# Kernel optimization log

Measured on AMD Instinct MI355X. Metric: run time of the kernel, lower is better.

Reference implementation:

```python
import jax, jax.numpy as jnp
import numpy as np

B, N, DIM, H, GH, DH, M, L, VOCAB = 2048, 15, 512, 8, 4, 64, 256, 12, 1024
FF_IN, FF_HID = 4096, 2048  # GLU: w1 512->4096 (chunk 2), w2 2048->512


def fixed_pos_emb(n, d):
    # performer_pytorch FixedPositionalEmbedding: cat(sin, cos) along feature dim
    inv_freq = 1.0 / (10000.0 ** (jnp.arange(0, d, 2, dtype=jnp.float32) / d))
    sinu = jnp.arange(n, dtype=jnp.float32)[:, None] * inv_freq[None, :]
    return jnp.concatenate([jnp.sin(sinu), jnp.cos(sinu)], axis=-1)  # [n, d]


def layernorm(x, g, b, eps=1e-5):
    mu = x.mean(-1, keepdims=True)
    var = x.var(-1, keepdims=True)
    return (x - mu) / jnp.sqrt(var + eps) * g + b


def pre_shift(x):
    # PreShiftTokens with shifts (-1, 0, 1); feats_per_shift = 512 // 3 = 170, remainder 2 dims untouched
    fps = x.shape[-1] // 3
    s0, s1, s2, rest = x[..., :fps], x[..., fps:2 * fps], x[..., 2 * fps:3 * fps], x[..., 3 * fps:]
    pad = jnp.zeros_like(s0[:, :1])
    left = jnp.concatenate([s0[:, 1:], pad], axis=1)    # shift -1 (toward past)
    right = jnp.concatenate([pad, s2[:, :-1]], axis=1)  # shift +1
    return jnp.concatenate([left, s1, right, rest], axis=-1)


def rotate_every_two(x):
    x1, x2 = x[..., ::2], x[..., 1::2]
    return jnp.stack([-x2, x1], axis=-1).reshape(x.shape)


def apply_rotary_global(q, k, sinu):
    # performer_pytorch apply_rotary_pos_emb: sinu = cat(sin, cos); interleaved repeat
    dh = sinu.shape[-1]
    sin = jnp.repeat(sinu[:, :dh // 2], 2, axis=-1)
    cos = jnp.repeat(sinu[:, dh // 2:], 2, axis=-1)
    rot = lambda t: t * cos + rotate_every_two(t) * sin
    return rot(q), rot(k)


def softmax_kernel(x, proj, is_query, eps=1e-4):
    # FAVOR+ positive random features for softmax kernel
    d = x.shape[-1]
    dn = d ** -0.25
    ratio = proj.shape[0] ** -0.5
    dash = jnp.einsum('bhnd,md->bhnm', x * dn, proj)
    diag = 0.5 * (dn ** 2) * jnp.sum(x * x, axis=-1, keepdims=True)
    if is_query:
        mx = jnp.max(dash, axis=-1, keepdims=True)
    else:
        mx = jnp.max(dash, axis=(-1, -2), keepdims=True)
    return ratio * (jnp.exp(dash - diag - mx) + eps)


def linear_attention(q, k, v):
    # non-causal O(n) attention: q,k are [b,h,n,m] features, v [b,h,n,e]
    k_sum = k.sum(axis=-2)
    d_inv = 1.0 / jnp.einsum('bhnm,bhm->bhn', q, k_sum)
    ctx = jnp.einsum('bhnm,bhne->bhme', k, v)
    return jnp.einsum('bhme,bhnm,bhn->bhne', ctx, q, d_inv)


def local_rotary(q, k):
    # local-attention lib SinusoidalEmbeddings + rotate_half convention
    d, n = q.shape[-1], q.shape[-2]
    inv_freq = 1.0 / (10000.0 ** (jnp.arange(0, d, 2, dtype=jnp.float32) / d))
    freqs = jnp.arange(n, dtype=jnp.float32)[:, None] * inv_freq[None, :]
    freqs = jnp.concatenate([freqs, freqs], axis=-1)  # [n, d]
    cos, sin = jnp.cos(freqs), jnp.sin(freqs)
    def rot_half(x):
        x1, x2 = x[..., :d // 2], x[..., d // 2:]
        return jnp.concatenate([-x2, x1], axis=-1)
    rot = lambda t: t * cos + rot_half(t) * sin
    return rot(q), rot(k)


def self_attention(x, wq, wk, wv, wo, bo, proj, sinu):
    b, n, _ = x.shape
    to_heads = lambda W: jnp.einsum('bnd,de->bne', x, W).reshape(b, n, H, DH).transpose(0, 2, 1, 3)
    q, k, v = to_heads(wq), to_heads(wk), to_heads(wv)
    # global (FAVOR+) heads first, then local heads
    qg, kg, vg = q[:, :GH], k[:, :GH], v[:, :GH]
    ql, kl, vl = q[:, GH:], k[:, GH:], v[:, GH:]
    qg, kg = apply_rotary_global(qg, kg, sinu)
    qp = softmax_kernel(qg, proj, True)
    kp = softmax_kernel(kg, proj, False)
    out_g = linear_attention(qp, kp, vg)
    # local attention: window 256 >= n=15 and bidirectional => exact softmax over real tokens
    ql, kl = local_rotary(ql, kl)
    sim = jnp.einsum('bhid,bhjd->bhij', ql, kl) * (DH ** -0.5)
    out_l = jnp.einsum('bhij,bhjd->bhid', jax.nn.softmax(sim, axis=-1), vl)
    out = jnp.concatenate([out_g, out_l], axis=1).transpose(0, 2, 1, 3).reshape(b, n, H * DH)
    return jnp.einsum('bnd,de->bne', out, wo) + bo


def glu_ff(x, w1, b1, w2, b2):
    h = jnp.einsum('bnd,df->bnf', x, w1) + b1
    a, g = jnp.split(h, 2, axis=-1)
    return jnp.einsum('bnf,fd->bnd', jax.nn.gelu(a, approximate=False) * g, w2) + b2


def _forward(x_mcc, token_emb, ln1_g, ln1_b, Wq, Wk, Wv, Wo, bo, proj,
             ln2_g, ln2_b, W1, b1, W2, b2, lnf_g, lnf_b, Wout, bout,
             Wl1, bl1, Wl2, bl2):
    b, n = x_mcc.shape
    x = token_emb[x_mcc] + fixed_pos_emb(n, DIM)[None]  # token + absolute sinusoidal emb
    sinu = fixed_pos_emb(n, DH)                          # per-layer rotary table

    def step(carry, p):
        x1, x2 = carry
        g1, be1, wq, wk, wv, wo, bo_, pr, g2, be2, w1, bf1, w2, bf2 = p
        # reversible block: y1 = x1 + f(x2); y2 = x2 + g(y1); f/g = LN -> token-shift -> fn
        y1 = x1 + self_attention(pre_shift(layernorm(x2, g1, be1)), wq, wk, wv, wo, bo_, pr, sinu)
        y2 = x2 + glu_ff(pre_shift(layernorm(y1, g2, be2)), w1, bf1, w2, bf2)
        return (y1, y2), None

    (x1, x2), _ = jax.lax.scan(
        step, (x, x),
        (ln1_g, ln1_b, Wq, Wk, Wv, Wo, bo, proj, ln2_g, ln2_b, W1, b1, W2, b2))
    x = x1 + x2  # ReversibleSequence: sum of the two streams
    x = layernorm(x, lnf_g, lnf_b)
    logits = jnp.einsum('bnd,dv->bnv', x, Wout) + bout  # [B, N, VOCAB]
    xa = logits.mean(axis=1)
    h = jax.nn.relu(xa @ Wl1 + bl1)
    return h @ Wl2 + bl2  # [B, 2]


def _gaussian_orth(m, d, rng):
    # gaussian_orthogonal_random_matrix with scaling=0
    blocks = []
    for _ in range(m // d + 1):
        qm, _ = np.linalg.qr(rng.standard_normal((d, d)))
        blocks.append(qm.T)
    mat = np.concatenate(blocks, axis=0)[:m]
    mult = np.linalg.norm(rng.standard_normal((m, d)), axis=1)
    return (mult[:, None] * mat).astype(np.float32)


def setup_inputs():
    key = jax.random.key(0)
    ks = jax.random.split(key, 16)
    s = 0.02
    rng = np.random.default_rng(0)
    proj = jnp.asarray(np.stack([_gaussian_orth(M, DH, rng) for _ in range(L)]))
    inp = {
        'x_mcc': jax.random.randint(ks[0], (B, N), 0, VOCAB, dtype=jnp.int32).astype(jnp.int64) if False else jax.random.randint(ks[0], (B, N), 0, VOCAB),
        'token_emb': jax.random.normal(ks[1], (VOCAB, DIM), jnp.float32) * s,
        'ln1_g': jnp.ones((L, DIM), jnp.float32),
        'ln1_b': jnp.zeros((L, DIM), jnp.float32),
        'Wq': jax.random.normal(ks[2], (L, DIM, H * DH), jnp.float32) * s,
        'Wk': jax.random.normal(ks[3], (L, DIM, H * DH), jnp.float32) * s,
        'Wv': jax.random.normal(ks[4], (L, DIM, H * DH), jnp.float32) * s,
        'Wo': jax.random.normal(ks[5], (L, H * DH, DIM), jnp.float32) * s,
        'bo': jnp.zeros((L, DIM), jnp.float32),
        'proj': proj,
        'ln2_g': jnp.ones((L, DIM), jnp.float32),
        'ln2_b': jnp.zeros((L, DIM), jnp.float32),
        'W1': jax.random.normal(ks[6], (L, DIM, FF_IN), jnp.float32) * s,
        'b1': jnp.zeros((L, FF_IN), jnp.float32),
        'W2': jax.random.normal(ks[7], (L, FF_HID, DIM), jnp.float32) * s,
        'b2': jnp.zeros((L, DIM), jnp.float32),
        'lnf_g': jnp.ones((DIM,), jnp.float32),
        'lnf_b': jnp.zeros((DIM,), jnp.float32),
        'Wout': jax.random.normal(ks[8], (DIM, VOCAB), jnp.float32) * s,
        'bout': jnp.zeros((VOCAB,), jnp.float32),
        'Wl1': jax.random.normal(ks[9], (VOCAB, 64), jnp.float32) * s,
        'bl1': jnp.zeros((64,), jnp.float32),
        'Wl2': jax.random.normal(ks[10], (64, 2), jnp.float32) * s,
        'bl2': jnp.zeros((2,), jnp.float32),
    }
    return inp


def reference(x_mcc, token_emb, ln1_g, ln1_b, Wq, Wk, Wv, Wo, bo, proj,
              ln2_g, ln2_b, W1, b1, W2, b2, lnf_g, lnf_b, Wout, bout,
              Wl1, bl1, Wl2, bl2):
    return _forward(x_mcc, token_emb, ln1_g, ln1_b, Wq, Wk, Wv, Wo, bo, proj,
                    ln2_g, ln2_b, W1, b1, W2, b2, lnf_g, lnf_b, Wout, bout,
                    Wl1, bl1, Wl2, bl2)
```

## Files before the change

kernel.cpp:

```cpp
#include <hip/hip_runtime.h>
#include <math.h>

#define BB 2048
#define NN 15
#define DIMM 512
#define NH 8
#define GHH 4
#define DHH 64
#define MF 256
#define NLAYERS 12
#define NVOCAB 1024
#define ROWS (BB*NN)
#define RT (ROWS/128)

typedef __attribute__((ext_vector_type(8))) short s8b;
typedef __attribute__((ext_vector_type(4))) short s4b;
typedef __attribute__((ext_vector_type(4))) float f4;
typedef unsigned short ushort;
typedef unsigned int uint;

__device__ __forceinline__ ushort f2b(float f) {
    uint u = __builtin_bit_cast(uint, f);
    u = u + 0x7FFF + ((u >> 16) & 1);
    return (ushort)(u >> 16);
}
__device__ __forceinline__ float b2f(ushort b) {
    return __builtin_bit_cast(float, (uint)b << 16);
}
__device__ __forceinline__ void gll16(const ushort* g, ushort* l) {
    __builtin_amdgcn_global_load_lds(
        (const __attribute__((address_space(1))) uint*)g,
        (__attribute__((address_space(3))) uint*)l, 16, 0, 0);
}

__global__ __launch_bounds__(256) void k_embed(const int* __restrict__ xm,
                                               const float* __restrict__ emb,
                                               float* __restrict__ x1,
                                               float* __restrict__ x2) {
    int idx = blockIdx.x * 256 + threadIdx.x;
    int row = idx >> 9;
    int d   = idx & 511;
    int n   = row % NN;
    int tok = xm[row];
    int j   = d & 255;
    float invf = expf(-(float)j * (9.2103403720f / 256.f));
    float arg  = (float)n * invf;
    float pe   = (d < 256) ? sinf(arg) : cosf(arg);
    float val  = emb[tok * DIMM + d] + pe;
    x1[idx] = val;
    x2[idx] = val;
}

template<int SHIFT, int ADD>
__global__ __launch_bounds__(256) void k_ln(const float* __restrict__ src,
                                            const float* __restrict__ src2,
                                            const float* __restrict__ gg,
                                            const float* __restrict__ bb,
                                            ushort* __restrict__ dst) {
    __shared__ float buf[NN][DIMM];
    int b    = blockIdx.x;
    int tid  = threadIdx.x;
    int wid  = tid >> 6;
    int lane = tid & 63;

    for (int n = wid; n < NN; n += 4) {
        size_t base = ((size_t)(b * NN + n)) * DIMM;
        float4 v0 = *(const float4*)(src + base + lane * 8);
        float4 v1 = *(const float4*)(src + base + lane * 8 + 4);
        if (ADD) {
            float4 w0 = *(const float4*)(src2 + base + lane * 8);
            float4 w1 = *(const float4*)(src2 + base + lane * 8 + 4);
            v0.x += w0.x; v0.y += w0.y; v0.z += w0.z; v0.w += w0.w;
            v1.x += w1.x; v1.y += w1.y; v1.z += w1.z; v1.w += w1.w;
        }
        float s = v0.x + v0.y + v0.z + v0.w + v1.x + v1.y + v1.z + v1.w;
        #pragma unroll
        for (int m = 1; m < 64; m <<= 1) s += __shfl_xor(s, m);
        float mu = s * (1.f / DIMM);
        float a0 = v0.x - mu, a1 = v0.y - mu, a2 = v0.z - mu, a3 = v0.w - mu;
        float a4 = v1.x - mu, a5 = v1.y - mu, a6 = v1.z - mu, a7 = v1.w - mu;
        float s2 = a0*a0 + a1*a1 + a2*a2 + a3*a3 + a4*a4 + a5*a5 + a6*a6 + a7*a7;
        #pragma unroll
        for (int m = 1; m < 64; m <<= 1) s2 += __shfl_xor(s2, m);
        float rstd = 1.f / sqrtf(s2 * (1.f / DIMM) + 1e-5f);
        float o[8] = {a0, a1, a2, a3, a4, a5, a6, a7};
        int d0 = lane * 8;
        #pragma unroll
        for (int i = 0; i < 8; ++i) {
            float val = o[i] * rstd * gg[d0 + i] + bb[d0 + i];
            if (SHIFT) buf[n][d0 + i] = val;
            else       dst[base + d0 + i] = f2b(val);
        }
    }
    if (SHIFT) {
        __syncthreads();
        for (int idx = tid; idx < NN * DIMM; idx += 256) {
            int n = idx >> 9, d = idx & 511;
            float val;
            if (d < 170)      val = (n < NN - 1) ? buf[n + 1][d] : 0.f;
            else if (d < 340) val = buf[n][d];
            else if (d < 510) val = (n > 0) ? buf[n - 1][d] : 0.f;
            else              val = buf[n][d];
            dst[((size_t)(b * NN + n)) * DIMM + d] = f2b(val);
        }
    }
}

__global__ __launch_bounds__(256) void k_wt(const float* __restrict__ src,
                                            ushort* __restrict__ dst, int K, int N) {
    __shared__ float t[32][33];
    int n0 = blockIdx.x * 32, k0 = blockIdx.y * 32;
    int tx = threadIdx.x & 31, ty = threadIdx.x >> 5;
    #pragma unroll
    for (int i = 0; i < 32; i += 8)
        t[ty + i][tx] = src[(size_t)(k0 + ty + i) * N + n0 + tx];
    __syncthreads();
    #pragma unroll
    for (int i = 0; i < 32; i += 8)
        dst[(size_t)(n0 + ty + i) * K + k0 + tx] = f2b(t[tx][ty + i]);
}

__global__ __launch_bounds__(256) void k_projcvt(const float* __restrict__ src,
                                                 ushort* __restrict__ dst, int n) {
    int i = blockIdx.x * 256 + threadIdx.x;
    if (i < n) dst[i] = f2b(src[i]);
}

template<int OUTB, int BIAS, int RES>
__global__ __launch_bounds__(256) void k_mm(const ushort* __restrict__ A,
                                            const ushort* __restrict__ Bt,
                                            const float* __restrict__ bias,
                                            const float* __restrict__ res,
                                            void* __restrict__ outv,
                                            int lda, int ldb, int K, int ldo) {
    __shared__ ushort smA[128 * 32];
    __shared__ ushort smB[128 * 32];
    int tid = threadIdx.x, wid = tid >> 6, lane = tid & 63;
    int row0 = blockIdx.x * 128, col0 = blockIdx.y * 128;
    int trow = tid >> 2, tkk = (tid & 3) * 8;
    f4 acc[4][4] = {};
    int rw = (wid >> 1) * 64, cw = (wid & 1) * 64;

    for (int k0 = 0; k0 < K; k0 += 32) {
        #pragma unroll
        for (int r = 0; r < 2; ++r) {
            gll16(A  + (size_t)(row0 + r * 64 + trow) * lda + k0 + tkk, smA + (r * 256 + wid * 64) * 8);
            gll16(Bt + (size_t)(col0 + r * 64 + trow) * ldb + k0 + tkk, smB + (r * 256 + wid * 64) * 8);
        }
        __syncthreads();
        s8b af[4], bf[4];
        #pragma unroll
        for (int m = 0; m < 4; ++m)
            af[m] = *(const s8b*)(smA + (rw + m * 16 + (lane & 15)) * 32 + (lane >> 4) * 8);
        #pragma unroll
        for (int n = 0; n < 4; ++n)
            bf[n] = *(const s8b*)(smB + (cw + n * 16 + (lane & 15)) * 32 + (lane >> 4) * 8);
        #pragma unroll
        for (int m = 0; m < 4; ++m)
            #pragma unroll
            for (int n = 0; n < 4; ++n)
                acc[m][n] = __builtin_amdgcn_mfma_f32_16x16x32_bf16(af[m], bf[n], acc[m][n], 0, 0, 0);
        __syncthreads();
    }
    #pragma unroll
    for (int m = 0; m < 4; ++m) {
        #pragma unroll
        for (int n = 0; n < 4; ++n) {
            int c = col0 + cw + n * 16 + (lane & 15);
            #pragma unroll
            for (int j = 0; j < 4; ++j) {
                int r = row0 + rw + m * 16 + (lane >> 4) * 4 + j;
                float v = acc[m][n][j];
                if (BIAS) v += bias[c];
                if (RES)  v += res[(size_t)r * ldo + c];
                if (OUTB) ((ushort*)outv)[(size_t)r * ldo + c] = f2b(v);
                else      ((float*)outv)[(size_t)r * ldo + c] = v;
            }
        }
    }
}

__global__ __launch_bounds__(256) void k_glu(const ushort* __restrict__ A,
                                             const ushort* __restrict__ Ba,
                                             const ushort* __restrict__ Bg,
                                             const float* __restrict__ ba,
                                             const float* __restrict__ bg,
                                             ushort* __restrict__ outp) {
    __shared__ ushort smA[128 * 32];
    __shared__ ushort smBa[128 * 32];
    __shared__ ushort smBg[128 * 32];
    int tid = threadIdx.x, wid = tid >> 6, lane = tid & 63;
    int row0 = blockIdx.x * 128, col0 = blockIdx.y * 128;
    int trow = tid >> 2, tkk = (tid & 3) * 8;
    f4 acca[4][4] = {}, accg[4][4] = {};
    int rw = (wid >> 1) * 64, cw = (wid & 1) * 64;

    for (int k0 = 0; k0 < 512; k0 += 32) {
        #pragma unroll
        for (int r = 0; r < 2; ++r) {
            gll16(A  + (size_t)(row0 + r * 64 + trow) * 512 + k0 + tkk, smA  + (r * 256 + wid * 64) * 8);
            gll16(Ba + (size_t)(col0 + r * 64 + trow) * 512 + k0 + tkk, smBa + (r * 256 + wid * 64) * 8);
            gll16(Bg + (size_t)(col0 + r * 64 + trow) * 512 + k0 + tkk, smBg + (r * 256 + wid * 64) * 8);
        }
        __syncthreads();
        s8b af[4], bfa[4], bfg[4];
        #pragma unroll
        for (int m = 0; m < 4; ++m)
            af[m] = *(const s8b*)(smA + (rw + m * 16 + (lane & 15)) * 32 + (lane >> 4) * 8);
        #pragma unroll
        for (int n = 0; n < 4; ++n) {
            bfa[n] = *(const s8b*)(smBa + (cw + n * 16 + (lane & 15)) * 32 + (lane >> 4) * 8);
            bfg[n] = *(const s8b*)(smBg + (cw + n * 16 + (lane & 15)) * 32 + (lane >> 4) * 8);
        }
        #pragma unroll
        for (int m = 0; m < 4; ++m)
            #pragma unroll
            for (int n = 0; n < 4; ++n) {
                acca[m][n] = __builtin_amdgcn_mfma_f32_16x16x32_bf16(af[m], bfa[n], acca[m][n], 0, 0, 0);
                accg[m][n] = __builtin_amdgcn_mfma_f32_16x16x32_bf16(af[m], bfg[n], accg[m][n], 0, 0, 0);
            }
        __syncthreads();
    }
    #pragma unroll
    for (int m = 0; m < 4; ++m) {
        #pragma unroll
        for (int n = 0; n < 4; ++n) {
            int c = col0 + cw + n * 16 + (lane & 15);
            float biasa = ba[c], biasg = bg[c];
            #pragma unroll
            for (int j = 0; j < 4; ++j) {
                int r = row0 + rw + m * 16 + (lane >> 4) * 4 + j;
                float a = acca[m][n][j] + biasa;
                float g = accg[m][n][j] + biasg;
                float ge = 0.5f * a * (1.f + erff(a * 0.70710678118f));
                outp[(size_t)r * 1024 + c] = f2b(ge * g);
            }
        }
    }
}

__global__ __launch_bounds__(256) void k_attng(const ushort* __restrict__ qkv,
                                               const ushort* __restrict__ projb,
                                               ushort* __restrict__ outp) {
    __shared__ ushort sxq[16][72];
    __shared__ ushort sxk[16][72];
    __shared__ ushort sVT[64][40];
    __shared__ ushort sqp[16][264];
    __shared__ ushort skp[16][264];
    __shared__ ushort sA[16][40];
    __shared__ float sdq[16], sdk[16], sdinv[16];
    __shared__ float sPq[4][16];
    __shared__ float sPk[4];
    int b = blockIdx.x, h = blockIdx.y;
    int tid = threadIdx.x, w = tid >> 6, l = tid & 63;
    int i16 = l & 15, g = l >> 4;
    const ushort* basep = qkv + (size_t)b * NN * 1536 + h * 64;

    {
        uint* z1 = (uint*)&sVT[0][0];
        for (int i = tid; i < 1280; i += 256) z1[i] = 0;
        uint* z2 = (uint*)&sA[0][0];
        for (int i = tid; i < 320; i += 256) z2[i] = 0;
        if (tid < 64) { sxq[15][tid] = 0; sxk[15][tid] = 0; }
    }
    __syncthreads();
    for (int idx = tid; idx < NN * 32; idx += 256) {
        int n = idx >> 5, i = idx & 31;
        float invf = expf(-(float)i * (9.2103403720f / 32.f));
        float cc = cosf((float)n * invf), ss = sinf((float)n * invf);
        float q0 = b2f(basep[n * 1536 + 2 * i]), q1 = b2f(basep[n * 1536 + 2 * i + 1]);
        sxq[n][2 * i]     = f2b(q0 * cc - q1 * ss);
        sxq[n][2 * i + 1] = f2b(q1 * cc + q0 * ss);
        float k0 = b2f(basep[n * 1536 + 512 + 2 * i]), k1 = b2f(basep[n * 1536 + 512 + 2 * i + 1]);
        sxk[n][2 * i]     = f2b(k0 * cc - k1 * ss);
        sxk[n][2 * i + 1] = f2b(k1 * cc + k0 * ss);
    }
    for (int idx = tid; idx < NN * 64; idx += 256) {
        int n = idx >> 6, e = idx & 63;
        sVT[e][n] = basep[n * 1536 + 1024 + e];
    }
    __syncthreads();
    if (w == 0) {
        int n = l >> 2, c = l & 3;
        float sa = 0.f, sb = 0.f;
        #pragma unroll
        for (int s = 0; s < 2; ++s) {
            s8b vq = *(const s8b*)&sxq[n][c * 16 + s * 8];
            s8b vk = *(const s8b*)&sxk[n][c * 16 + s * 8];
            #pragma unroll
            for (int j = 0; j < 8; ++j) {
                float x = b2f((ushort)vq[j]); sa += x * x;
                float y = b2f((ushort)vk[j]); sb += y * y;
            }
        }
        sa += __shfl_xor(sa, 1); sa += __shfl_xor(sa, 2);
        sb += __shfl_xor(sb, 1); sb += __shfl_xor(sb, 2);
        if (c == 0) { sdq[n] = 0.0625f * sa; sdk[n] = 0.0625f * sb; }
    }
    s8b bq[2], bk[2];
    bq[0] = *(const s8b*)&sxq[i16][g * 8];
    bq[1] = *(const s8b*)&sxq[i16][32 + g * 8];
    bk[0] = *(const s8b*)&sxk[i16][g * 8];
    bk[1] = *(const s8b*)&sxk[i16][32 + g * 8];
    f4 accq[4] = {}, acck[4] = {};
    const ushort* pb = projb + (size_t)(w * 64 + i16) * 64 + g * 8;
    #pragma unroll
    for (int mi = 0; mi < 4; ++mi) {
        #pragma unroll
        for (int ks = 0; ks < 2; ++ks) {
            s8b a = *(const s8b*)(pb + mi * 16 * 64 + ks * 32);
            accq[mi] = __builtin_amdgcn_mfma_f32_16x16x32_bf16(a, bq[ks], accq[mi], 0, 0, 0);
            acck[mi] = __builtin_amdgcn_mfma_f32_16x16x32_bf16(a, bk[ks], acck[mi], 0, 0, 0);
        }
    }
    float mq = -1e30f, mkv = -1e30f;
    #pragma unroll
    for (int mi = 0; mi < 4; ++mi)
        #pragma unroll
        for (int j = 0; j < 4; ++j) {
            mq  = fmaxf(mq, accq[mi][j]);
            mkv = fmaxf(mkv, acck[mi][j]);
        }
    if (i16 == 15) mkv = -1e30f;
    mq = fmaxf(mq, __shfl_xor(mq, 16));
    mq = fmaxf(mq, __shfl_xor(mq, 32));
    #pragma unroll
    for (int m = 1; m < 64; m <<= 1) mkv = fmaxf(mkv, __shfl_xor(mkv, m));
    if (l < 16) sPq[w][l] = mq;
    if (l == 0) sPk[w] = mkv;
    __syncthreads();
    float mxq = fmaxf(fmaxf(sPq[0][i16], sPq[1][i16]), fmaxf(sPq[2][i16], sPq[3][i16]));
    float mxk = fmaxf(fmaxf(sPk[0], sPk[1]), fmaxf(sPk[2], sPk[3]));
    const float dn = 0.35355339059f;
    float dgq = sdq[i16], dgk = sdk[i16];
    #pragma unroll
    for (int mi = 0; mi < 4; ++mi) {
        s4b pq, pk;
        #pragma unroll
        for (int j = 0; j < 4; ++j) {
            float vq = 0.0625f * (expf(dn * (accq[mi][j] - mxq) - dgq) + 1e-4f);
            float vk = 0.0625f * (expf(dn * (acck[mi][j] - mxk) - dgk) + 1e-4f);
            pq[j] = (short)f2b(vq);
            pk[j] = (short)f2b(vk);
        }
        int m0 = (w * 4 + mi) * 16 + g * 4;
        *(s4b*)&sqp[i16][m0] = pq;
        *(s4b*)&skp[i16][m0] = pk;
    }
    __syncthreads();
    if (w == 0) {
        f4 accA = {};
        #pragma unroll
        for (int ks = 0; ks < 8; ++ks) {
            s8b aq = *(const s8b*)&sqp[i16][ks * 32 + g * 8];
            s8b ak = *(const s8b*)&skp[i16][ks * 32 + g * 8];
            accA = __builtin_amdgcn_mfma_f32_16x16x32_bf16(aq, ak, accA, 0, 0, 0);
        }
        #pragma unroll
        for (int j = 0; j < 4; ++j) {
            float v = (i16 == 15) ? 0.f : accA[j];
            float s = v;
            s += __shfl_xor(s, 1); s += __shfl_xor(s, 2);
            s += __shfl_xor(s, 4); s += __shfl_xor(s, 8);
            sA[g * 4 + j][i16] = f2b(v);
            if (i16 == 0) sdinv[g * 4 + j] = 1.f / s;
        }
    }
    __syncthreads();
    {
        s8b aA = *(const s8b*)&sA[i16][g * 8];
        s8b bV = *(const s8b*)&sVT[w * 16 + i16][g * 8];
        f4 z = {};
        f4 o = __builtin_amdgcn_mfma_f32_16x16x32_bf16(aA, bV, z, 0, 0, 0);
        #pragma unroll
        for (int j = 0; j < 4; ++j) {
            int n = g * 4 + j;
            if (n < NN)
                outp[((size_t)(b * NN + n)) * DIMM + h * 64 + w * 16 + i16] = f2b(o[j] * sdinv[n]);
        }
    }
}

__global__ __launch_bounds__(64) void k_attnl(const ushort* __restrict__ qkv,
                                              ushort* __restrict__ outp) {
    __shared__ ushort sxq[16][72];
    __shared__ ushort sxk[16][72];
    __shared__ ushort sVT[64][40];
    __shared__ ushort sA[16][40];
    __shared__ float sdinv[16];
    int b = blockIdx.x, h = blockIdx.y + GHH;
    int l = threadIdx.x;
    int i16 = l & 15, g = l >> 4;
    const ushort* basep = qkv + (size_t)b * NN * 1536 + h * 64;

    {
        uint* z1 = (uint*)&sVT[0][0];
        for (int i = l; i < 1280; i += 64) z1[i] = 0;
        uint* z2 = (uint*)&sA[0][0];
        for (int i = l; i < 320; i += 64) z2[i] = 0;
        sxq[15][l] = 0; sxk[15][l] = 0;
    }
    __syncthreads();
    for (int idx = l; idx < NN * 32; idx += 64) {
        int n = idx >> 5, i = idx & 31;
        float invf = expf(-(float)i * (9.2103403720f / 32.f));
        float cc = cosf((float)n * invf), ss = sinf((float)n * invf);
        float qlo = b2f(basep[n * 1536 + i]), qhi = b2f(basep[n * 1536 + i + 32]);
        sxq[n][i]      = f2b(qlo * cc - qhi * ss);
        sxq[n][i + 32] = f2b(qhi * cc + qlo * ss);
        float klo = b2f(basep[n * 1536 + 512 + i]), khi = b2f(basep[n * 1536 + 512 + i + 32]);
        sxk[n][i]      = f2b(klo * cc - khi * ss);
        sxk[n][i + 32] = f2b(khi * cc + klo * ss);
    }
    for (int idx = l; idx < NN * 64; idx += 64) {
        int n = idx >> 6, e = idx & 63;
        sVT[e][n] = basep[n * 1536 + 1024 + e];
    }
    __syncthreads();
    f4 acc = {};
    #pragma unroll
    for (int ks = 0; ks < 2; ++ks) {
        s8b aq = *(const s8b*)&sxq[i16][ks * 32 + g * 8];
        s8b bk = *(const s8b*)&sxk[i16][ks * 32 + g * 8];
        acc = __builtin_amdgcn_mfma_f32_16x16x32_bf16(aq, bk, acc, 0, 0, 0);
    }
    #pragma unroll
    for (int j = 0; j < 4; ++j) {
        float v = (i16 == 15) ? -1e30f : acc[j] * 0.125f;
        float mx = v;
        mx = fmaxf(mx, __shfl_xor(mx, 1));
        mx = fmaxf(mx, __shfl_xor(mx, 2));
        mx = fmaxf(mx, __shfl_xor(mx, 4));
        mx = fmaxf(mx, __shfl_xor(mx, 8));
        float e = (i16 == 15) ? 0.f : expf(v - mx);
        float s = e;
        s += __shfl_xor(s, 1); s += __shfl_xor(s, 2);
        s += __shfl_xor(s, 4); s += __shfl_xor(s, 8);
        sA[g * 4 + j][i16] = f2b(e);
        if (i16 == 0) sdinv[g * 4 + j] = 1.f / s;
    }
    __syncthreads();
    s8b aA = *(const s8b*)&sA[i16][g * 8];
    #pragma unroll
    for (int et = 0; et < 4; ++et) {
        s8b bV = *(const s8b*)&sVT[et * 16 + i16][g * 8];
        f4 z = {};
        f4 o = __builtin_amdgcn_mfma_f32_16x16x32_bf16(aA, bV, z, 0, 0, 0);
        #pragma unroll
        for (int j = 0; j < 4; ++j) {
            int n = g * 4 + j;
            if (n < NN)
                outp[((size_t)(b * NN + n)) * DIMM + h * 64 + et * 16 + i16] = f2b(o[j] * sdinv[n]);
        }
    }
}

__global__ __launch_bounds__(256) void k_head(const float* __restrict__ logits,
                                              const float* __restrict__ Wl1,
                                              const float* __restrict__ bl1,
                                              const float* __restrict__ Wl2,
                                              const float* __restrict__ bl2,
                                              float* __restrict__ outp) {
    __shared__ float xa[NVOCAB];
    __shared__ float hh[64];
    int b = blockIdx.x, tid = threadIdx.x;
    for (int c = tid; c < NVOCAB; c += 256) {
        float s = 0.f;
        #pragma unroll
        for (int n = 0; n < NN; ++n) s += logits[((size_t)(b * NN + n)) * NVOCAB + c];
        xa[c] = s * (1.f / NN);
    }
    __syncthreads();
    if (tid < 64) {
        float s = bl1[tid];
        for (int kk = 0; kk < NVOCAB; ++kk) s += xa[kk] * Wl1[kk * 64 + tid];
        hh[tid] = fmaxf(s, 0.f);
    }
    __syncthreads();
    if (tid < 2) {
        float s = bl2[tid];
        #pragma unroll
        for (int j = 0; j < 64; ++j) s += hh[j] * Wl2[j * 2 + tid];
        outp[(size_t)b * 2 + tid] = s;
    }
}

extern "C" void kernel_launch(void* const* d_in, const int* in_sizes, int n_in,
                              void* d_out, int out_size, void* d_ws, size_t ws_size,
                              hipStream_t stream) {
    (void)in_sizes; (void)n_in; (void)out_size; (void)ws_size;
    const int*   x_mcc = (const int*)d_in[0];
    const float* emb   = (const float*)d_in[1];
    const float* ln1g  = (const float*)d_in[2];
    const float* ln1b  = (const float*)d_in[3];
    const float* Wq    = (const float*)d_in[4];
    const float* Wk    = (const float*)d_in[5];
    const float* Wv    = (const float*)d_in[6];
    const float* Wo    = (const float*)d_in[7];
    const float* bo    = (const float*)d_in[8];
    const float* proj  = (const float*)d_in[9];
    const float* ln2g  = (const float*)d_in[10];
    const float* ln2b  = (const float*)d_in[11];
    const float* W1    = (const float*)d_in[12];
    const float* b1    = (const float*)d_in[13];
    const float* W2    = (const float*)d_in[14];
    const float* b2    = (const float*)d_in[15];
    const float* lnfg  = (const float*)d_in[16];
    const float* lnfb  = (const float*)d_in[17];
    const float* Wout  = (const float*)d_in[18];
    const float* bout  = (const float*)d_in[19];
    const float* Wl1   = (const float*)d_in[20];
    const float* bl1   = (const float*)d_in[21];
    const float* Wl2   = (const float*)d_in[22];
    const float* bl2   = (const float*)d_in[23];
    float* outp = (float*)d_out;

    char* ws = (char*)d_ws;
    const size_t S = (size_t)ROWS * DIMM * 4;
    float*  x1   = (float*)(ws);
    float*  x2   = (float*)(ws + S);
    ushort* xs   = (ushort*)(ws + 2 * S);
    ushort* qkv  = (ushort*)(ws + 2 * S + S / 2);
    ushort* ub   = (ushort*)(ws + 4 * S);
    ushort* wb   = (ushort*)(ws + 5 * S);
    float*  logits = (float*)(ws + 2 * S + S / 2);
    ushort* qkvT = wb;
    ushort* woT  = wb + 1536 * 512;
    ushort* w1T  = wb + 1536 * 512 + 512 * 512;
    ushort* w2T  = w1T + 4096 * 512;
    ushort* projb = w2T + 512 * 2048;
    ushort* woutT = w1T;

    k_embed<<<(ROWS * DIMM) / 256, 256, 0, stream>>>(x_mcc, emb, x1, x2);
    k_projcvt<<<(NLAYERS * MF * DHH) / 256, 256, 0, stream>>>(proj, projb, NLAYERS * MF * DHH);

    for (int l = 0; l < NLAYERS; ++l) {
        const size_t w512 = (size_t)l * 512 * 512;
        k_wt<<<dim3(16, 16), 256, 0, stream>>>(Wq + w512, qkvT,              512, 512);
        k_wt<<<dim3(16, 16), 256, 0, stream>>>(Wk + w512, qkvT + 512 * 512,  512, 512);
        k_wt<<<dim3(16, 16), 256, 0, stream>>>(Wv + w512, qkvT + 1024 * 512, 512, 512);
        k_wt<<<dim3(16, 16), 256, 0, stream>>>(Wo + w512, woT, 512, 512);
        k_wt<<<dim3(128, 16), 256, 0, stream>>>(W1 + (size_t)l * 512 * 4096, w1T, 512, 4096);
        k_wt<<<dim3(16, 64), 256, 0, stream>>>(W2 + (size_t)l * 2048 * 512, w2T, 2048, 512);

        k_ln<1, 0><<<BB, 256, 0, stream>>>(x2, nullptr, ln1g + l * DIMM, ln1b + l * DIMM, xs);
        k_mm<1, 0, 0><<<dim3(RT, 12), 256, 0, stream>>>(xs, qkvT, nullptr, nullptr, qkv, 512, 512, 512, 1536);
        k_attng<<<dim3(BB, GHH), 256, 0, stream>>>(qkv, projb + (size_t)l * MF * DHH, xs);
        k_attnl<<<dim3(BB, NH - GHH), 64, 0, stream>>>(qkv, xs);
        k_mm<0, 1, 1><<<dim3(RT, 4), 256, 0, stream>>>(xs, woT, bo + l * DIMM, x1, x1, 512, 512, 512, 512);
        k_ln<1, 0><<<BB, 256, 0, stream>>>(x1, nullptr, ln2g + l * DIMM, ln2b + l * DIMM, xs);
        k_glu<<<dim3(RT, 8), 256, 0, stream>>>(xs, w1T, w1T + (size_t)2048 * 512,
                                               b1 + (size_t)l * 4096, b1 + (size_t)l * 4096 + 2048, ub);
        k_mm<0, 1, 1><<<dim3(RT, 4), 256, 0, stream>>>(ub, w2T, b2 + l * DIMM, x2, x2, 1024, 2048, 1024, 512);
        k_glu<<<dim3(RT, 8), 256, 0, stream>>>(xs, w1T + (size_t)1024 * 512, w1T + (size_t)3072 * 512,
                                               b1 + (size_t)l * 4096 + 1024, b1 + (size_t)l * 4096 + 3072, ub);
        k_mm<0, 0, 1><<<dim3(RT, 4), 256, 0, stream>>>(ub, w2T + 1024, nullptr, x2, x2, 1024, 2048, 1024, 512);
    }

    k_ln<0, 1><<<BB, 256, 0, stream>>>(x1, x2, lnfg, lnfb, xs);
    k_wt<<<dim3(32, 16), 256, 0, stream>>>(Wout, woutT, 512, 1024);
    k_mm<0, 1, 0><<<dim3(RT, 8), 256, 0, stream>>>(xs, woutT, bout, nullptr, logits, 512, 512, 512, 1024);
    k_head<<<BB, 256, 0, stream>>>(logits, Wl1, bl1, Wl2, bl2, outp);
}
```

Before: 9.754 ms.

## Double-buffer LDS in GEMM and GLU kernels and halve N tile to 64

The k_mm and k_glu kernels now keep two LDS stages and issue the global-to-LDS loads for the next K slice before running the MFMAs on the current slice. This is meant to hide load latency behind compute. The column tile shrinks from 128 to 64 and launch bounds request more resident blocks per CU, doubling the grid in y to raise occupancy. The cost is lower reuse of A per block, so A is read from global memory twice as often. The loop keeps a single barrier per iteration.

```diff
diff --git a/kernel.cpp b/kernel.cpp
--- a/kernel.cpp
+++ b/kernel.cpp
@@ -127,49 +127,56 @@
 }
 
 template<int OUTB, int BIAS, int RES>
-__global__ __launch_bounds__(256) void k_mm(const ushort* __restrict__ A,
-                                            const ushort* __restrict__ Bt,
-                                            const float* __restrict__ bias,
-                                            const float* __restrict__ res,
-                                            void* __restrict__ outv,
-                                            int lda, int ldb, int K, int ldo) {
-    __shared__ ushort smA[128 * 32];
-    __shared__ ushort smB[128 * 32];
+__global__ __launch_bounds__(256, 3) void k_mm(const ushort* __restrict__ A,
+                                               const ushort* __restrict__ Bt,
+                                               const float* __restrict__ bias,
+                                               const float* __restrict__ res,
+                                               void* __restrict__ outv,
+                                               int lda, int ldb, int K, int ldo) {
+    __shared__ ushort smA[2][128 * 32];
+    __shared__ ushort smB[2][64 * 32];
     int tid = threadIdx.x, wid = tid >> 6, lane = tid & 63;
-    int row0 = blockIdx.x * 128, col0 = blockIdx.y * 128;
-    int trow = tid >> 2, tkk = (tid & 3) * 8;
-    f4 acc[4][4] = {};
-    int rw = (wid >> 1) * 64, cw = (wid & 1) * 64;
-
-    for (int k0 = 0; k0 < K; k0 += 32) {
-        #pragma unroll
-        for (int r = 0; r < 2; ++r) {
-            gll16(A  + (size_t)(row0 + r * 64 + trow) * lda + k0 + tkk, smA + (r * 256 + wid * 64) * 8);
-            gll16(Bt + (size_t)(col0 + r * 64 + trow) * ldb + k0 + tkk, smB + (r * 256 + wid * 64) * 8);
-        }
-        __syncthreads();
-        s8b af[4], bf[4];
+    int i16 = lane & 15, g = lane >> 4;
+    int row0 = blockIdx.x * 128, col0 = blockIdx.y * 64;
+    int wr = wid >> 1, wc = wid & 1;
+    f4 acc[4][2] = {};
+    const int seg0 = wid * 64 + lane;
+    const int seg1 = 256 + seg0;
+    const int NT = K >> 5;
+
+    auto STAGE = [&](int c, int k0) {
+        gll16(A  + (size_t)(row0 + (seg0 >> 2)) * lda + k0 + (seg0 & 3) * 8, &smA[c][(wid * 64) * 8]);
+        gll16(A  + (size_t)(row0 + (seg1 >> 2)) * lda + k0 + (seg1 & 3) * 8, &smA[c][(256 + wid * 64) * 8]);
+        gll16(Bt + (size_t)(col0 + (seg0 >> 2)) * ldb + k0 + (seg0 & 3) * 8, &smB[c][(wid * 64) * 8]);
+    };
+
+    STAGE(0, 0);
+    __syncthreads();
+    for (int t = 0; t < NT; ++t) {
+        int cur = t & 1;
+        if (t + 1 < NT) STAGE(cur ^ 1, (t + 1) * 32);
+        s8b af[4], bf[2];
         #pragma unroll
         for (int m = 0; m < 4; ++m)
-            af[m] = *(const s8b*)(smA + (rw + m * 16 + (lane & 15)) * 32 + (lane >> 4) * 8);
-        #pragma unroll
-        for (int n = 0; n < 4; ++n)
-            bf[n] = *(const s8b*)(smB + (cw + n * 16 + (lane & 15)) * 32 + (lane >> 4) * 8);
+            af[m] = *(const s8b*)&smA[cur][(wr * 64 + m * 16 + i16) * 32 + g * 8];
+        #pragma unroll
+        for (int n = 0; n < 2; ++n)
+            bf[n] = *(const s8b*)&smB[cur][(wc * 32 + n * 16 + i16) * 32 + g * 8];
         #pragma unroll
         for (int m = 0; m < 4; ++m)
             #pragma unroll
-            for (int n = 0; n < 4; ++n)
+            for (int n = 0; n < 2; ++n)
                 acc[m][n] = __builtin_amdgcn_mfma_f32_16x16x32_bf16(af[m], bf[n], acc[m][n], 0, 0, 0);
         __syncthreads();
     }
     #pragma unroll
     for (int m = 0; m < 4; ++m) {
         #pragma unroll
-        for (int n = 0; n < 4; ++n) {
-            int c = col0 + cw + n * 16 + (lane & 15);
+        for (int n = 0; n < 2; ++n) {
+            int c = col0 + wc * 32 + n * 16 + i16;
             #pragma unroll
             for (int j = 0; j < 4; ++j) {
-                int r = row0 + rw + m * 16 + (lane >> 4) * 4 + j;
+                int r = row0 + wr * 64 + m * 16 + g * 4 + j;
                 float v = acc[m][n][j];
                 if (BIAS) v += bias[c];
                 if (RES)  v += res[(size_t)r * ldo + c];
@@ -180,42 +187,48 @@
     }
 }
 
-__global__ __launch_bounds__(256) void k_glu(const ushort* __restrict__ A,
-                                             const ushort* __restrict__ Ba,
-                                             const ushort* __restrict__ Bg,
-                                             const float* __restrict__ ba,
-                                             const float* __restrict__ bg,
-                                             ushort* __restrict__ outp) {
-    __shared__ ushort smA[128 * 32];
-    __shared__ ushort smBa[128 * 32];
-    __shared__ ushort smBg[128 * 32];
+__global__ __launch_bounds__(256, 2) void k_glu(const ushort* __restrict__ A,
+                                                const ushort* __restrict__ Ba,
+                                                const ushort* __restrict__ Bg,
+                                                const float* __restrict__ ba,
+                                                const float* __restrict__ bg,
+                                                ushort* __restrict__ outp) {
+    __shared__ ushort smA[2][128 * 32];
+    __shared__ ushort smBa[2][64 * 32];
+    __shared__ ushort smBg[2][64 * 32];
     int tid = threadIdx.x, wid = tid >> 6, lane = tid & 63;
-    int row0 = blockIdx.x * 128, col0 = blockIdx.y * 128;
-    int trow = tid >> 2, tkk = (tid & 3) * 8;
-    f4 acca[4][4] = {}, accg[4][4] = {};
-    int rw = (wid >> 1) * 64, cw = (wid & 1) * 64;
-
-    for (int k0 = 0; k0 < 512; k0 += 32) {
-        #pragma unroll
-        for (int r = 0; r < 2; ++r) {
-            gll16(A  + (size_t)(row0 + r * 64 + trow) * 512 + k0 + tkk, smA  + (r * 256 + wid * 64) * 8);
-            gll16(Ba + (size_t)(col0 + r * 64 + trow) * 512 + k0 + tkk, smBa + (r * 256 + wid * 64) * 8);
-            gll16(Bg + (size_t)(col0 + r * 64 + trow) * 512 + k0 + tkk, smBg + (r * 256 + wid * 64) * 8);
-        }
-        __syncthreads();
-        s8b af[4], bfa[4], bfg[4];
+    int i16 = lane & 15, g = lane >> 4;
+    int row0 = blockIdx.x * 128, col0 = blockIdx.y * 64;
+    int wr = wid >> 1, wc = wid & 1;
+    f4 acca[4][2] = {}, accg[4][2] = {};
+    const int seg0 = wid * 64 + lane;
+    const int seg1 = 256 + seg0;
+
+    auto STAGE = [&](int c, int k0) {
+        gll16(A  + (size_t)(row0 + (seg0 >> 2)) * 512 + k0 + (seg0 & 3) * 8, &smA[c][(wid * 64) * 8]);
+        gll16(A  + (size_t)(row0 + (seg1 >> 2)) * 512 + k0 + (seg1 & 3) * 8, &smA[c][(256 + wid * 64) * 8]);
+        gll16(Ba + (size_t)(col0 + (seg0 >> 2)) * 512 + k0 + (seg0 & 3) * 8, &smBa[c][(wid * 64) * 8]);
+        gll16(Bg + (size_t)(col0 + (seg0 >> 2)) * 512 + k0 + (seg0 & 3) * 8, &smBg[c][(wid * 64) * 8]);
+    };
+
+    STAGE(0, 0);
+    __syncthreads();
+    for (int t = 0; t < 16; ++t) {
+        int cur = t & 1;
+        if (t + 1 < 16) STAGE(cur ^ 1, (t + 1) * 32);
+        s8b af[4], bfa[2], bfg[2];
         #pragma unroll
         for (int m = 0; m < 4; ++m)
-            af[m] = *(const s8b*)(smA + (rw + m * 16 + (lane & 15)) * 32 + (lane >> 4) * 8);
-        #pragma unroll
-        for (int n = 0; n < 4; ++n) {
-            bfa[n] = *(const s8b*)(smBa + (cw + n * 16 + (lane & 15)) * 32 + (lane >> 4) * 8);
-            bfg[n] = *(const s8b*)(smBg + (cw + n * 16 + (lane & 15)) * 32 + (lane >> 4) * 8);
+            af[m] = *(const s8b*)&smA[cur][(wr * 64 + m * 16 + i16) * 32 + g * 8];
+        #pragma unroll
+        for (int n = 0; n < 2; ++n) {
+            bfa[n] = *(const s8b*)&smBa[cur][(wc * 32 + n * 16 + i16) * 32 + g * 8];
+            bfg[n] = *(const s8b*)&smBg[cur][(wc * 32 + n * 16 + i16) * 32 + g * 8];
         }
         #pragma unroll
         for (int m = 0; m < 4; ++m)
             #pragma unroll
-            for (int n = 0; n < 4; ++n) {
+            for (int n = 0; n < 2; ++n) {
                 acca[m][n] = __builtin_amdgcn_mfma_f32_16x16x32_bf16(af[m], bfa[n], acca[m][n], 0, 0, 0);
                 accg[m][n] = __builtin_amdgcn_mfma_f32_16x16x32_bf16(af[m], bfg[n], accg[m][n], 0, 0, 0);
             }
@@ -224,16 +237,16 @@
     #pragma unroll
     for (int m = 0; m < 4; ++m) {
         #pragma unroll
-        for (int n = 0; n < 4; ++n) {
-            int c = col0 + cw + n * 16 + (lane & 15);
+        for (int n = 0; n < 2; ++n) {
+            int c = col0 + wc * 32 + n * 16 + i16;
             float biasa = ba[c], biasg = bg[c];
             #pragma unroll
             for (int j = 0; j < 4; ++j) {
-                int r = row0 + rw + m * 16 + (lane >> 4) * 4 + j;
+                int r = row0 + wr * 64 + m * 16 + g * 4 + j;
                 float a = acca[m][n][j] + biasa;
-                float g = accg[m][n][j] + biasg;
+                float gg = accg[m][n][j] + biasg;
                 float ge = 0.5f * a * (1.f + erff(a * 0.70710678118f));
-                outp[(size_t)r * 1024 + c] = f2b(ge * g);
+                outp[(size_t)r * 1024 + c] = f2b(ge * gg);
             }
         }
     }
@@ -544,21 +557,21 @@
         k_wt<<<dim3(16, 64), 256, 0, stream>>>(W2 + (size_t)l * 2048 * 512, w2T, 2048, 512);
 
         k_ln<1, 0><<<BB, 256, 0, stream>>>(x2, nullptr, ln1g + l * DIMM, ln1b + l * DIMM, xs);
-        k_mm<1, 0, 0><<<dim3(RT, 12), 256, 0, stream>>>(xs, qkvT, nullptr, nullptr, qkv, 512, 512, 512, 1536);
+        k_mm<1, 0, 0><<<dim3(RT, 24), 256, 0, stream>>>(xs, qkvT, nullptr, nullptr, qkv, 512, 512, 512, 1536);
         k_attng<<<dim3(BB, GHH), 256, 0, stream>>>(qkv, projb + (size_t)l * MF * DHH, xs);
         k_attnl<<<dim3(BB, NH - GHH), 64, 0, stream>>>(qkv, xs);
-        k_mm<0, 1, 1><<<dim3(RT, 4), 256, 0, stream>>>(xs, woT, bo + l * DIMM, x1, x1, 512, 512, 512, 512);
+        k_mm<0, 1, 1><<<dim3(RT, 8), 256, 0, stream>>>(xs, woT, bo + l * DIMM, x1, x1, 512, 512, 512, 512);
         k_ln<1, 0><<<BB, 256, 0, stream>>>(x1, nullptr, ln2g + l * DIMM, ln2b + l * DIMM, xs);
-        k_glu<<<dim3(RT, 8), 256, 0, stream>>>(xs, w1T, w1T + (size_t)2048 * 512,
-                                               b1 + (size_t)l * 4096, b1 + (size_t)l * 4096 + 2048, ub);
-        k_mm<0, 1, 1><<<dim3(RT, 4), 256, 0, stream>>>(ub, w2T, b2 + l * DIMM, x2, x2, 1024, 2048, 1024, 512);
-        k_glu<<<dim3(RT, 8), 256, 0, stream>>>(xs, w1T + (size_t)1024 * 512, w1T + (size_t)3072 * 512,
-                                               b1 + (size_t)l * 4096 + 1024, b1 + (size_t)l * 4096 + 3072, ub);
-        k_mm<0, 0, 1><<<dim3(RT, 4), 256, 0, stream>>>(ub, w2T + 1024, nullptr, x2, x2, 1024, 2048, 1024, 512);
+        k_glu<<<dim3(RT, 16), 256, 0, stream>>>(xs, w1T, w1T + (size_t)2048 * 512,
+                                                b1 + (size_t)l * 4096, b1 + (size_t)l * 4096 + 2048, ub);
+        k_mm<0, 1, 1><<<dim3(RT, 8), 256, 0, stream>>>(ub, w2T, b2 + l * DIMM, x2, x2, 1024, 2048, 1024, 512);
+        k_glu<<<dim3(RT, 16), 256, 0, stream>>>(xs, w1T + (size_t)1024 * 512, w1T + (size_t)3072 * 512,
+                                                b1 + (size_t)l * 4096 + 1024, b1 + (size_t)l * 4096 + 3072, ub);
+        k_mm<0, 0, 1><<<dim3(RT, 8), 256, 0, stream>>>(ub, w2T + 1024, nullptr, x2, x2, 1024, 2048, 1024, 512);
     }
 
     k_ln<0, 1><<<BB, 256, 0, stream>>>(x1, x2, lnfg, lnfb, xs);
     k_wt<<<dim3(32, 16), 256, 0, stream>>>(Wout, woutT, 512, 1024);
-    k_mm<0, 1, 0><<<dim3(RT, 8), 256, 0, stream>>>(xs, woutT, bout, nullptr, logits, 512, 512, 512, 1024);
+    k_mm<0, 1, 0><<<dim3(RT, 16), 256, 0, stream>>>(xs, woutT, bout, nullptr, logits, 512, 512, 512, 1024);
     k_head<<<BB, 256, 0, stream>>>(logits, Wl1, bl1, Wl2, bl2, outp);
 }
```

Result: faster. 8.266 ms (-15.3%).

## Double-buffer GEMM LDS tiles and fuse GLU halves via interleaved W1 packing

Applied to the files above, without the earlier changes.

GEMM and GLU kernels now double-buffer their shared-memory tiles, prefetching the next K slice while computing the current one, and drop one barrier per iteration. W1 is repacked with value and gate columns interleaved, so one full-width GLU kernel pairs them through a lane shuffle. A single K=2048 FF2 GEMM replaces two half GEMMs plus two GLU launches. This doubles LDS use per block, which may lower occupancy, and the GLU epilogue leaves half the lanes idle on stores.

```diff
diff --git a/kernel.cpp b/kernel.cpp
--- a/kernel.cpp
+++ b/kernel.cpp
@@ -120,6 +120,23 @@
         dst[(size_t)(n0 + ty + i) * K + k0 + tx] = f2b(t[tx][ty + i]);
 }
 
+__global__ __launch_bounds__(256) void k_wtp(const float* __restrict__ src,
+                                             ushort* __restrict__ dst) {
+    __shared__ float t[32][33];
+    int c0 = blockIdx.x * 32, k0 = blockIdx.y * 32;
+    int tx = threadIdx.x & 31, ty = threadIdx.x >> 5;
+    #pragma unroll
+    for (int i = 0; i < 32; i += 8)
+        t[ty + i][tx] = src[(size_t)(k0 + ty + i) * 4096 + c0 + tx];
+    __syncthreads();
+    #pragma unroll
+    for (int i = 0; i < 32; i += 8) {
+        int c = c0 + ty + i;
+        int rr = (c < 2048) ? 2 * c : 2 * (c - 2048) + 1;
+        dst[(size_t)rr * 512 + k0 + tx] = f2b(t[tx][ty + i]);
+    }
+}
+
 __global__ __launch_bounds__(256) void k_projcvt(const float* __restrict__ src,
                                                  ushort* __restrict__ dst, int n) {
     int i = blockIdx.x * 256 + threadIdx.x;
@@ -133,28 +150,35 @@
                                             const float* __restrict__ res,
                                             void* __restrict__ outv,
                                             int lda, int ldb, int K, int ldo) {
-    __shared__ ushort smA[128 * 32];
-    __shared__ ushort smB[128 * 32];
+    __shared__ ushort smA[2][128 * 32];
+    __shared__ ushort smB[2][128 * 32];
     int tid = threadIdx.x, wid = tid >> 6, lane = tid & 63;
+    int i16 = lane & 15, g = lane >> 4;
     int row0 = blockIdx.x * 128, col0 = blockIdx.y * 128;
+    int rw = (wid >> 1) * 64, cw = (wid & 1) * 64;
     int trow = tid >> 2, tkk = (tid & 3) * 8;
     f4 acc[4][4] = {};
-    int rw = (wid >> 1) * 64, cw = (wid & 1) * 64;
-
-    for (int k0 = 0; k0 < K; k0 += 32) {
-        #pragma unroll
-        for (int r = 0; r < 2; ++r) {
-            gll16(A  + (size_t)(row0 + r * 64 + trow) * lda + k0 + tkk, smA + (r * 256 + wid * 64) * 8);
-            gll16(Bt + (size_t)(col0 + r * 64 + trow) * ldb + k0 + tkk, smB + (r * 256 + wid * 64) * 8);
-        }
-        __syncthreads();
+    const int NT = K >> 5;
+
+    auto STAGE = [&](int c, int k0) {
+        gll16(A  + (size_t)(row0 + trow) * lda + k0 + tkk,      &smA[c][tid * 8]);
+        gll16(A  + (size_t)(row0 + 64 + trow) * lda + k0 + tkk, &smA[c][2048 + tid * 8]);
+        gll16(Bt + (size_t)(col0 + trow) * ldb + k0 + tkk,      &smB[c][tid * 8]);
+        gll16(Bt + (size_t)(col0 + 64 + trow) * ldb + k0 + tkk, &smB[c][2048 + tid * 8]);
+    };
+
+    STAGE(0, 0);
+    __syncthreads();
+    for (int t = 0; t < NT; ++t) {
+        int cur = t & 1;
+        if (t + 1 < NT) STAGE(cur ^ 1, (t + 1) * 32);
         s8b af[4], bf[4];
         #pragma unroll
         for (int m = 0; m < 4; ++m)
-            af[m] = *(const s8b*)(smA + (rw + m * 16 + (lane & 15)) * 32 + (lane >> 4) * 8);
+            af[m] = *(const s8b*)&smA[cur][(rw + m * 16 + i16) * 32 + g * 8];
         #pragma unroll
         for (int n = 0; n < 4; ++n)
-            bf[n] = *(const s8b*)(smB + (cw + n * 16 + (lane & 15)) * 32 + (lane >> 4) * 8);
+            bf[n] = *(const s8b*)&smB[cur][(cw + n * 16 + i16) * 32 + g * 8];
         #pragma unroll
         for (int m = 0; m < 4; ++m)
             #pragma unroll
@@ -166,10 +190,10 @@
     for (int m = 0; m < 4; ++m) {
         #pragma unroll
         for (int n = 0; n < 4; ++n) {
-            int c = col0 + cw + n * 16 + (lane & 15);
+            int c = col0 + cw + n * 16 + i16;
             #pragma unroll
             for (int j = 0; j < 4; ++j) {
-                int r = row0 + rw + m * 16 + (lane >> 4) * 4 + j;
+                int r = row0 + rw + m * 16 + g * 4 + j;
                 float v = acc[m][n][j];
                 if (BIAS) v += bias[c];
                 if (RES)  v += res[(size_t)r * ldo + c];
@@ -180,60 +204,61 @@
     }
 }
 
-__global__ __launch_bounds__(256) void k_glu(const ushort* __restrict__ A,
-                                             const ushort* __restrict__ Ba,
-                                             const ushort* __restrict__ Bg,
-                                             const float* __restrict__ ba,
-                                             const float* __restrict__ bg,
-                                             ushort* __restrict__ outp) {
-    __shared__ ushort smA[128 * 32];
-    __shared__ ushort smBa[128 * 32];
-    __shared__ ushort smBg[128 * 32];
+__global__ __launch_bounds__(256) void k_glup(const ushort* __restrict__ A,
+                                              const ushort* __restrict__ Bp,
+                                              const float* __restrict__ b1l,
+                                              ushort* __restrict__ outp) {
+    __shared__ ushort smA[2][128 * 32];
+    __shared__ ushort smB[2][128 * 32];
     int tid = threadIdx.x, wid = tid >> 6, lane = tid & 63;
+    int i16 = lane & 15, g = lane >> 4;
     int row0 = blockIdx.x * 128, col0 = blockIdx.y * 128;
+    int rw = (wid >> 1) * 64, cw = (wid & 1) * 64;
     int trow = tid >> 2, tkk = (tid & 3) * 8;
-    f4 acca[4][4] = {}, accg[4][4] = {};
-    int rw = (wid >> 1) * 64, cw = (wid & 1) * 64;
-
-    for (int k0 = 0; k0 < 512; k0 += 32) {
-        #pragma unroll
-        for (int r = 0; r < 2; ++r) {
-            gll16(A  + (size_t)(row0 + r * 64 + trow) * 512 + k0 + tkk, smA  + (r * 256 + wid * 64) * 8);
-            gll16(Ba + (size_t)(col0 + r * 64 + trow) * 512 + k0 + tkk, smBa + (r * 256 + wid * 64) * 8);
-            gll16(Bg + (size_t)(col0 + r * 64 + trow) * 512 + k0 + tkk, smBg + (r * 256 + wid * 64) * 8);
-        }
-        __syncthreads();
-        s8b af[4], bfa[4], bfg[4];
+    f4 acc[4][4] = {};
+
+    auto STAGE = [&](int c, int k0) {
+        gll16(A  + (size_t)(row0 + trow) * 512 + k0 + tkk,      &smA[c][tid * 8]);
+        gll16(A  + (size_t)(row0 + 64 + trow) * 512 + k0 + tkk, &smA[c][2048 + tid * 8]);
+        gll16(Bp + (size_t)(col0 + trow) * 512 + k0 + tkk,      &smB[c][tid * 8]);
+        gll16(Bp + (size_t)(col0 + 64 + trow) * 512 + k0 + tkk, &smB[c][2048 + tid * 8]);
+    };
+
+    STAGE(0, 0);
+    __syncthreads();
+    for (int t = 0; t < 16; ++t) {
+        int cur = t & 1;
+        if (t + 1 < 16) STAGE(cur ^ 1, (t + 1) * 32);
+        s8b af[4], bf[4];
         #pragma unroll
         for (int m = 0; m < 4; ++m)
-            af[m] = *(const s8b*)(smA + (rw + m * 16 + (lane & 15)) * 32 + (lane >> 4) * 8);
-        #pragma unroll
-        for (int n = 0; n < 4; ++n) {
-            bfa[n] = *(const s8b*)(smBa + (cw + n * 16 + (lane & 15)) * 32 + (lane >> 4) * 8);
-            bfg[n] = *(const s8b*)(smBg + (cw + n * 16 + (lane & 15)) * 32 + (lane >> 4) * 8);
-        }
+            af[m] = *(const s8b*)&smA[cur][(rw + m * 16 + i16) * 32 + g * 8];
+        #pragma unroll
+        for (int n = 0; n < 4; ++n)
+            bf[n] = *(const s8b*)&smB[cur][(cw + n * 16 + i16) * 32 + g * 8];
         #pragma unroll
         for (int m = 0; m < 4; ++m)
             #pragma unroll
-            for (int n = 0; n < 4; ++n) {
-                acca[m][n] = __builtin_amdgcn_mfma_f32_16x16x32_bf16(af[m], bfa[n], acca[m][n], 0, 0, 0);
-                accg[m][n] = __builtin_amdgcn_mfma_f32_16x16x32_bf16(af[m], bfg[n], accg[m][n], 0, 0, 0);
-            }
+            for (int n = 0; n < 4; ++n)
+                acc[m][n] = __builtin_amdgcn_mfma_f32_16x16x32_bf16(af[m], bf[n], acc[m][n], 0, 0, 0);
         __syncthreads();
     }
     #pragma unroll
     for (int m = 0; m < 4; ++m) {
         #pragma unroll
         for (int n = 0; n < 4; ++n) {
-            int c = col0 + cw + n * 16 + (lane & 15);
-            float biasa = ba[c], biasg = bg[c];
+            int c = col0 + cw + n * 16 + i16;
+            int p = c >> 1;
+            float bv = b1l[(c & 1) * 2048 + p];
             #pragma unroll
             for (int j = 0; j < 4; ++j) {
-                int r = row0 + rw + m * 16 + (lane >> 4) * 4 + j;
-                float a = acca[m][n][j] + biasa;
-                float g = accg[m][n][j] + biasg;
-                float ge = 0.5f * a * (1.f + erff(a * 0.70710678118f));
-                outp[(size_t)r * 1024 + c] = f2b(ge * g);
+                int r = row0 + rw + m * 16 + g * 4 + j;
+                float v = acc[m][n][j] + bv;
+                float w = __shfl_xor(v, 1);
+                if (!(c & 1)) {
+                    float ge = 0.5f * v * (1.f + erff(v * 0.70710678118f));
+                    outp[(size_t)r * 2048 + p] = f2b(ge * w);
+                }
             }
         }
     }
@@ -521,15 +546,15 @@
     float*  x2   = (float*)(ws + S);
     ushort* xs   = (ushort*)(ws + 2 * S);
     ushort* qkv  = (ushort*)(ws + 2 * S + S / 2);
-    ushort* ub   = (ushort*)(ws + 4 * S);
+    ushort* ub   = (ushort*)(ws + 2 * S + S / 2);
+    float*  logits = (float*)(ws + 2 * S + S / 2);
     ushort* wb   = (ushort*)(ws + 5 * S);
-    float*  logits = (float*)(ws + 2 * S + S / 2);
     ushort* qkvT = wb;
     ushort* woT  = wb + 1536 * 512;
-    ushort* w1T  = wb + 1536 * 512 + 512 * 512;
-    ushort* w2T  = w1T + 4096 * 512;
+    ushort* w1p  = wb + 1536 * 512 + 512 * 512;
+    ushort* w2T  = w1p + 4096 * 512;
     ushort* projb = w2T + 512 * 2048;
-    ushort* woutT = w1T;
+    ushort* woutT = w1p;
 
     k_embed<<<(ROWS * DIMM) / 256, 256, 0, stream>>>(x_mcc, emb, x1, x2);
     k_projcvt<<<(NLAYERS * MF * DHH) / 256, 256, 0, stream>>>(proj, projb, NLAYERS * MF * DHH);
@@ -540,7 +565,7 @@
         k_wt<<<dim3(16, 16), 256, 0, stream>>>(Wk + w512, qkvT + 512 * 512,  512, 512);
         k_wt<<<dim3(16, 16), 256, 0, stream>>>(Wv + w512, qkvT + 1024 * 512, 512, 512);
         k_wt<<<dim3(16, 16), 256, 0, stream>>>(Wo + w512, woT, 512, 512);
-        k_wt<<<dim3(128, 16), 256, 0, stream>>>(W1 + (size_t)l * 512 * 4096, w1T, 512, 4096);
+        k_wtp<<<dim3(128, 16), 256, 0, stream>>>(W1 + (size_t)l * 512 * 4096, w1p);
         k_wt<<<dim3(16, 64), 256, 0, stream>>>(W2 + (size_t)l * 2048 * 512, w2T, 2048, 512);
 
         k_ln<1, 0><<<BB, 256, 0, stream>>>(x2, nullptr, ln1g + l * DIMM, ln1b + l * DIMM, xs);
@@ -549,12 +574,8 @@
         k_attnl<<<dim3(BB, NH - GHH), 64, 0, stream>>>(qkv, xs);
         k_mm<0, 1, 1><<<dim3(RT, 4), 256, 0, stream>>>(xs, woT, bo + l * DIMM, x1, x1, 512, 512, 512, 512);
         k_ln<1, 0><<<BB, 256, 0, stream>>>(x1, nullptr, ln2g + l * DIMM, ln2b + l * DIMM, xs);
-        k_glu<<<dim3(RT, 8), 256, 0, stream>>>(xs, w1T, w1T + (size_t)2048 * 512,
-                                               b1 + (size_t)l * 4096, b1 + (size_t)l * 4096 + 2048, ub);
-        k_mm<0, 1, 1><<<dim3(RT, 4), 256, 0, stream>>>(ub, w2T, b2 + l * DIMM, x2, x2, 1024, 2048, 1024, 512);
-        k_glu<<<dim3(RT, 8), 256, 0, stream>>>(xs, w1T + (size_t)1024 * 512, w1T + (size_t)3072 * 512,
-                                               b1 + (size_t)l * 4096 + 1024, b1 + (size_t)l * 4096 + 3072, ub);
-        k_mm<0, 0, 1><<<dim3(RT, 4), 256, 0, stream>>>(ub, w2T + 1024, nullptr, x2, x2, 1024, 2048, 1024, 512);
+        k_glup<<<dim3(RT, 32), 256, 0, stream>>>(xs, w1p, b1 + (size_t)l * 4096, ub);
+        k_mm<0, 1, 1><<<dim3(RT, 4), 256, 0, stream>>>(ub, w2T, b2 + l * DIMM, x2, x2, 2048, 2048, 2048, 512);
     }
 
     k_ln<0, 1><<<BB, 256, 0, stream>>>(x1, x2, lnfg, lnfb, xs);
```

Result: faster. 7.912 ms (-18.9%).
